# Optimization experiments

Hardware: AMD Instinct MI355X
Metric: run time of the kernel (lower is better)

Reference implementation:

```python
import jax, jax.numpy as jnp
import numpy as np
import math
from jax import lax

# cfg['MODEL'] constants
MU = 0.1          # FISTA step size
LMBD = 0.1        # LAMBDA[0], sparsity weight
N_DICT = 1        # EXPANSION_FACTOR
N_STEPS = 6       # NUM_LAYERS (FISTA iterations)
K = 3             # kernel_size
PAD = 1           # padding
STRIDE = 1        # stride (POOLING=False, stride passed to conv)
DN = ('NCHW', 'OIHW', 'NCHW')


def _conv(x, w):
    # F.conv2d(x, w, stride=1, padding=PAD)
    return lax.conv_general_dilated(x, w, (STRIDE, STRIDE), [(PAD, PAD), (PAD, PAD)], dimension_numbers=DN)


def _conv_t(y, w):
    # F.conv_transpose2d(y, w, stride=1, padding=PAD) == conv2d with flipped, in/out-swapped kernel, pad K-1-PAD
    wt = jnp.transpose(jnp.flip(w, (-1, -2)), (1, 0, 2, 3))  # [Cin, Cout, K, K]
    p = K - 1 - PAD
    return lax.conv_general_dilated(y, wt, (1, 1), [(p, p), (p, p)], dimension_numbers=DN)


def _shrink(z, thr):
    # non_negative=True soft-threshold: relu(z - thr)
    return jax.nn.relu(z - thr)


def setup_inputs() -> dict:
    key = jax.random.key(0)
    k1, k2 = jax.random.split(key)
    x = jax.random.normal(k1, (16, 64, 56, 56), dtype=jnp.float32)
    # dictionary weight [out_channels, in_channels*n_dict, K, K], kaiming-ish scale
    W = jax.random.normal(k2, (128, 64 * N_DICT, K, K), dtype=jnp.float32) * 0.05
    return {"x": x, "W": W}


def reference(x, W):
    # w_norm: each output filter normalized to unit Frobenius norm
    Wn = W / jnp.sqrt(jnp.sum(W * W, axis=(1, 2, 3), keepdims=True) + 1e-12)
    thr = MU * LMBD
    xr = jnp.tile(x, (1, N_DICT, 1, 1)) if N_DICT > 1 else x

    # FISTA iteration 0: c = shrink(mu * D^T x)
    c = _shrink(MU * _conv(xr, Wn), thr)
    y = c
    c_prev = c
    t = 1.0
    for _ in range(N_STEPS - 1):
        r = xr - _conv_t(y, Wn)                       # residual x - D c
        c_new = _shrink(y + MU * _conv(r, Wn), thr)   # gradient step + shrink
        t_next = (1.0 + math.sqrt(1.0 + 4.0 * t * t)) / 2.0
        y = c_new + ((t - 1.0) / t_next) * (c_new - c_prev)  # momentum
        c_prev = c_new
        t = t_next
    # POOLING=False -> DictConv2d returns the sparse code directly
    return c_prev
```

## Files before the change

kernel.cpp:

```cpp
#include <hip/hip_runtime.h>
#include <hip/hip_bf16.h>
#include <math.h>

typedef __attribute__((ext_vector_type(8))) short short8;
typedef __attribute__((ext_vector_type(4))) float f32x4;

#define MU_  0.1f
#define THR_ 0.01f

static __device__ inline short f2bf(float f) {
    __hip_bfloat16 h = __float2bfloat16(f);
    return *reinterpret_cast<short*>(&h);
}
static __device__ inline float bf2f(unsigned short u) {
    unsigned int x = ((unsigned int)u) << 16;
    return __builtin_bit_cast(float, x);
}

__global__ __launch_bounds__(256) void zero_kernel(float4* p, int n4) {
    int i = blockIdx.x * 256 + threadIdx.x;
    if (i < n4) p[i] = make_float4(0.f, 0.f, 0.f, 0.f);
}

__global__ __launch_bounds__(64) void wnorm_pack(
    const float* __restrict__ W, short* __restrict__ Wf2, short* __restrict__ Wt2) {
    int co = blockIdx.x, ci = threadIdx.x;
    const float* wp = W + (co * 64 + ci) * 9;
    float v[9]; float s = 0.f;
#pragma unroll
    for (int t = 0; t < 9; ++t) { v[t] = wp[t]; s += v[t] * v[t]; }
#pragma unroll
    for (int off = 32; off; off >>= 1) s += __shfl_xor(s, off, 64);
    float inv = 1.0f / sqrtf(s + 1e-12f);
#pragma unroll
    for (int t = 0; t < 9; ++t) {
        Wf2[((t * 8 + (ci >> 3)) * 128 + co) * 8 + (ci & 7)] = f2bf(v[t] * inv);
        Wt2[((t * 16 + (co >> 3)) * 64 + ci) * 8 + (co & 7)] = f2bf(v[8 - t] * inv);
    }
}

__global__ __launch_bounds__(256) void pack_x(
    const float* __restrict__ x, short* __restrict__ Xp) {
    __shared__ float lx[64 * 57];
    int row = blockIdx.x, n = blockIdx.y, tid = threadIdx.x;
    short* dst = Xp + ((size_t)(n * 58 + row) * 68) * 64;
    if (row >= 1 && row <= 56) {
        int h = row - 1;
        for (int j = tid; j < 64 * 56; j += 256) {
            int ci = j / 56, w = j - ci * 56;
            lx[ci * 57 + w] = x[((size_t)(n * 64 + ci)) * 3136 + h * 56 + w];
        }
        __syncthreads();
        for (int j = tid; j < 68 * 64; j += 256) {
            int s = j >> 6, ci = j & 63;
            float val = (s >= 2 && s < 58) ? lx[ci * 57 + (s - 2)] : 0.f;
            dst[(s << 6) + (ci ^ ((s & 7) << 3))] = f2bf(val);
        }
    } else {
        for (int j = tid; j < 68 * 64; j += 256) dst[j] = 0;
    }
}

__global__ __launch_bounds__(256) void conv_fwd(
    const short* __restrict__ inp,
    const short* __restrict__ Wf2,
    short* __restrict__ Yp,
    short* __restrict__ Cp,
    float* __restrict__ outp, int mode, float beta) {
    __shared__ __align__(16) short smem[14688];
    const int r = blockIdx.x + 1, cb = blockIdx.y, n = blockIdx.z, tid = threadIdx.x;
    {
        const short8* src = (const short8*)(inp + ((size_t)(n * 58 + (r - 1)) * 68) * 64);
        for (int j = tid; j < 1632; j += 256) {
            int srow = j >> 3, w = j & 7;
            *(short8*)(smem + srow * 72 + w * 8) = src[j];
        }
    }
    const int lane = tid & 63, ct = tid >> 6, quad = lane >> 4, l15 = lane & 15;
    const int co = cb * 64 + ct * 16 + l15;

    short8 Areg[18];
#pragma unroll
    for (int f = 0; f < 18; ++f) {
        int t = f >> 1, half = f & 1;
        Areg[f] = *(const short8*)(Wf2 + ((size_t)((t * 8 + half * 4 + quad) * 128 + co)) * 8);
    }
    __syncthreads();

    f32x4 acc[4];
#pragma unroll
    for (int pt = 0; pt < 4; ++pt) acc[pt] = (f32x4){0.f, 0.f, 0.f, 0.f};

#pragma unroll
    for (int f = 0; f < 18; ++f) {
        const int t = f >> 1, half = f & 1;
        const int dh = t / 3, dw = t % 3;
        const int u = l15 + dw + 1;
        const int phys = (half * 4 + quad) ^ (u & 7);
        const int base = (dh * 68 + u) * 72 + phys * 8;
#pragma unroll
        for (int pt = 0; pt < 4; ++pt) {
            short8 bv = *(const short8*)(smem + base + pt * 1152);
            acc[pt] = __builtin_amdgcn_mfma_f32_16x16x32_bf16(Areg[f], bv, acc[pt], 0, 0, 0);
        }
    }

    __syncthreads();
    short* tb_y = smem;
    short* tb_c = smem + 4608;
    const size_t prow = ((size_t)(n * 58 + r) * 68) * 128;
    if (mode != 0) {
        for (int item = tid; item < 448; item += 256) {
            int vv = item >> 3, g = item & 7;
            int s = vv + 2;
            size_t off = prow + (size_t)s * 128 + 8 * ((g + 8 * cb) ^ (s & 7));
            int o = vv * 72 + 8 * (g ^ (vv & 3));
            *(short8*)(tb_y + o) = *(const short8*)(Yp + off);
            if (mode == 1) *(short8*)(tb_c + o) = *(const short8*)(Cp + off);
        }
    }
    __syncthreads();
    const int h = r - 1;
#pragma unroll
    for (int pt = 0; pt < 4; ++pt) {
        const int px = pt * 16 + l15;
#pragma unroll
        for (int reg = 0; reg < 4; ++reg) {
            const int lch = ct * 16 + quad * 4 + reg;
            const int slot = px * 72 + (lch ^ ((px & 3) << 3));
            const float a = acc[pt][reg];
            if (mode == 0) {
                float c = fmaxf(MU_ * a - THR_, 0.f);
                short cb16 = f2bf(c);
                tb_y[slot] = cb16;
                tb_c[slot] = cb16;
            } else if (mode == 1) {
                float yold = bf2f((unsigned short)tb_y[slot]);
                float cold = bf2f((unsigned short)tb_c[slot]);
                float c = fmaxf(yold + MU_ * a - THR_, 0.f);
                tb_y[slot] = f2bf(c + beta * (c - cold));
                tb_c[slot] = f2bf(c);
            } else {
                if (px < 56) {
                    float yold = bf2f((unsigned short)tb_y[slot]);
                    float c = fmaxf(yold + MU_ * a - THR_, 0.f);
                    outp[((size_t)(n * 128 + cb * 64 + lch)) * 3136 + h * 56 + px] = c;
                }
            }
        }
    }
    if (mode != 2) {
        __syncthreads();
        for (int item = tid; item < 448; item += 256) {
            int vv = item >> 3, g = item & 7;
            int so = vv * 72 + 8 * (g ^ (vv & 3));
            short8 yv = *(const short8*)(tb_y + so);
            short8 cv = *(const short8*)(tb_c + so);
            int s = vv + 2;
            size_t off = prow + (size_t)s * 128 + 8 * ((g + 8 * cb) ^ (s & 7));
            *(short8*)(Yp + off) = yv;
            *(short8*)(Cp + off) = cv;
        }
    }
}

__global__ __launch_bounds__(256) void conv_t(
    const short* __restrict__ Ypb,
    const short* __restrict__ Wt2,
    const short* __restrict__ Xp,
    short* __restrict__ Rp) {
    __shared__ __align__(16) short smem[14688];
    const int r = blockIdx.x + 1, n = blockIdx.y, tid = threadIdx.x;
    const int lane = tid & 63, ct = tid >> 6, quad = lane >> 4, l15 = lane & 15;
    const int ci = ct * 16 + l15;
    const short8* src = (const short8*)(Ypb + ((size_t)(n * 58 + (r - 1)) * 68) * 128);

    f32x4 acc[4];
#pragma unroll
    for (int pt = 0; pt < 4; ++pt) acc[pt] = (f32x4){0.f, 0.f, 0.f, 0.f};

#pragma unroll
    for (int p = 0; p < 2; ++p) {
        if (p) __syncthreads();
        for (int j = tid; j < 1632; j += 256) {
            int srow = j >> 3, w = j & 7;
            *(short8*)(smem + srow * 72 + w * 8) = src[srow * 16 + p * 8 + w];
        }
        short8 Areg[18];
#pragma unroll
        for (int f = 0; f < 18; ++f) {
            int t = f >> 1, sh = f & 1;
            Areg[f] = *(const short8*)(Wt2 +
                ((size_t)((t * 16 + (p * 2 + sh) * 4 + quad) * 64 + ci)) * 8);
        }
        __syncthreads();
#pragma unroll
        for (int f = 0; f < 18; ++f) {
            const int t = f >> 1, sh = f & 1;
            const int dh = t / 3, dw = t % 3;
            const int u = l15 + dw + 1;
            const int phys = (sh * 4 + quad) ^ (u & 7);
            const int base = (dh * 68 + u) * 72 + phys * 8;
#pragma unroll
            for (int pt = 0; pt < 4; ++pt) {
                short8 bv = *(const short8*)(smem + base + pt * 1152);
                acc[pt] = __builtin_amdgcn_mfma_f32_16x16x32_bf16(Areg[f], bv, acc[pt], 0, 0, 0);
            }
        }
    }

    __syncthreads();
    short* tb = smem;
    const size_t prow = ((size_t)(n * 58 + r) * 68) * 64;
    for (int item = tid; item < 448; item += 256) {
        int vv = item >> 3, g = item & 7;
        int s = vv + 2;
        *(short8*)(tb + vv * 72 + 8 * (g ^ (vv & 3))) =
            *(const short8*)(Xp + prow + (size_t)s * 64 + 8 * (g ^ (s & 7)));
    }
    __syncthreads();
#pragma unroll
    for (int pt = 0; pt < 4; ++pt) {
        const int px = pt * 16 + l15;
#pragma unroll
        for (int reg = 0; reg < 4; ++reg) {
            const int cir = ct * 16 + quad * 4 + reg;
            const int slot = px * 72 + (cir ^ ((px & 3) << 3));
            float xo = bf2f((unsigned short)tb[slot]);
            tb[slot] = f2bf(xo - acc[pt][reg]);
        }
    }
    __syncthreads();
    for (int item = tid; item < 448; item += 256) {
        int vv = item >> 3, g = item & 7;
        short8 val = *(const short8*)(tb + vv * 72 + 8 * (g ^ (vv & 3)));
        int s = vv + 2;
        *(short8*)(Rp + prow + (size_t)s * 64 + 8 * (g ^ (s & 7))) = val;
    }
}

extern "C" void kernel_launch(void* const* d_in, const int* in_sizes, int n_in,
                              void* d_out, int out_size, void* d_ws, size_t ws_size,
                              hipStream_t stream) {
    const float* x = (const float*)d_in[0];
    const float* W = (const float*)d_in[1];
    float* out = (float*)d_out;

    const size_t XPN = (size_t)16 * 58 * 68 * 64;
    const size_t YPN = 2 * XPN;
    short* Xp = (short*)d_ws;
    short* Rp = Xp + XPN;
    short* Yp = Rp + XPN;
    short* Cp = Yp + YPN;
    short* Wf2 = Cp + YPN;
    short* Wt2 = Wf2 + 73728;

    const int n4 = (int)((XPN + YPN) * 2 / 16);
    hipLaunchKernelGGL(zero_kernel, dim3((n4 + 255) / 256), dim3(256), 0, stream,
                       (float4*)Rp, n4);
    hipLaunchKernelGGL(wnorm_pack, dim3(128), dim3(64), 0, stream, W, Wf2, Wt2);
    hipLaunchKernelGGL(pack_x, dim3(58, 16), dim3(256), 0, stream, x, Xp);

    dim3 gf(56, 2, 16), gt(56, 16), b(256, 1, 1);
    hipLaunchKernelGGL(conv_fwd, gf, b, 0, stream, Xp, Wf2, Yp, Cp,
                       (float*)nullptr, 0, 0.f);
    double t = 1.0;
    for (int it = 1; it <= 5; ++it) {
        hipLaunchKernelGGL(conv_t, gt, b, 0, stream, Yp, Wt2, Xp, Rp);
        double tn = (1.0 + sqrt(1.0 + 4.0 * t * t)) / 2.0;
        float beta = (float)((t - 1.0) / tn);
        hipLaunchKernelGGL(conv_fwd, gf, b, 0, stream, Rp, Wf2, Yp, Cp,
                           (it == 5) ? out : (float*)nullptr, (it == 5) ? 2 : 1,
                           beta);
        t = tn;
    }
}
```

Measured before the change: 372.4 us.

## Process two output rows per block in convs and fuse prep kernels

Each conv_fwd and conv_t block now computes two output rows instead of one. It stages four input rows in shared memory so the three-row halo is shared between them, and the register-held weights are reused across both rows. The Y and X epilogue loads are issued before the MFMA loop so their latency overlaps compute. The zeroing, weight-normalisation and x-packing kernels are merged into one launch. The grid is halved, which cuts the occupancy available to hide latency, and the extra accumulators and shared memory increase register and LDS pressure.

```diff
diff --git a/kernel.cpp b/kernel.cpp
--- a/kernel.cpp
+++ b/kernel.cpp
@@ -17,47 +17,51 @@
     return __builtin_bit_cast(float, x);
 }
 
-__global__ __launch_bounds__(256) void zero_kernel(float4* p, int n4) {
-    int i = blockIdx.x * 256 + threadIdx.x;
-    if (i < n4) p[i] = make_float4(0.f, 0.f, 0.f, 0.f);
-}
-
-__global__ __launch_bounds__(64) void wnorm_pack(
-    const float* __restrict__ W, short* __restrict__ Wf2, short* __restrict__ Wt2) {
-    int co = blockIdx.x, ci = threadIdx.x;
-    const float* wp = W + (co * 64 + ci) * 9;
-    float v[9]; float s = 0.f;
-#pragma unroll
-    for (int t = 0; t < 9; ++t) { v[t] = wp[t]; s += v[t] * v[t]; }
-#pragma unroll
-    for (int off = 32; off; off >>= 1) s += __shfl_xor(s, off, 64);
-    float inv = 1.0f / sqrtf(s + 1e-12f);
-#pragma unroll
-    for (int t = 0; t < 9; ++t) {
-        Wf2[((t * 8 + (ci >> 3)) * 128 + co) * 8 + (ci & 7)] = f2bf(v[t] * inv);
-        Wt2[((t * 16 + (co >> 3)) * 64 + ci) * 8 + (co & 7)] = f2bf(v[8 - t] * inv);
-    }
-}
-
-__global__ __launch_bounds__(256) void pack_x(
-    const float* __restrict__ x, short* __restrict__ Xp) {
+#define ZB_ 5916
+
+__global__ __launch_bounds__(256) void prep_kernel(
+    const float* __restrict__ x, const float* __restrict__ W,
+    float4* __restrict__ zbase, int n4,
+    short* __restrict__ Xp, short* __restrict__ Wf2, short* __restrict__ Wt2) {
     __shared__ float lx[64 * 57];
-    int row = blockIdx.x, n = blockIdx.y, tid = threadIdx.x;
-    short* dst = Xp + ((size_t)(n * 58 + row) * 68) * 64;
-    if (row >= 1 && row <= 56) {
-        int h = row - 1;
-        for (int j = tid; j < 64 * 56; j += 256) {
-            int ci = j / 56, w = j - ci * 56;
-            lx[ci * 57 + w] = x[((size_t)(n * 64 + ci)) * 3136 + h * 56 + w];
-        }
-        __syncthreads();
-        for (int j = tid; j < 68 * 64; j += 256) {
-            int s = j >> 6, ci = j & 63;
-            float val = (s >= 2 && s < 58) ? lx[ci * 57 + (s - 2)] : 0.f;
-            dst[(s << 6) + (ci ^ ((s & 7) << 3))] = f2bf(val);
+    const int bid = blockIdx.x, tid = threadIdx.x;
+    if (bid < ZB_) {
+        int i = bid * 256 + tid;
+        if (i < n4) zbase[i] = make_float4(0.f, 0.f, 0.f, 0.f);
+    } else if (bid < ZB_ + 32) {
+        int co = (bid - ZB_) * 4 + (tid >> 6);
+        int ci = tid & 63;
+        const float* wp = W + (co * 64 + ci) * 9;
+        float v[9]; float s = 0.f;
+#pragma unroll
+        for (int t = 0; t < 9; ++t) { v[t] = wp[t]; s += v[t] * v[t]; }
+#pragma unroll
+        for (int off = 32; off; off >>= 1) s += __shfl_xor(s, off, 64);
+        float inv = 1.0f / sqrtf(s + 1e-12f);
+#pragma unroll
+        for (int t = 0; t < 9; ++t) {
+            Wf2[((t * 8 + (ci >> 3)) * 128 + co) * 8 + (ci & 7)] = f2bf(v[t] * inv);
+            Wt2[((t * 16 + (co >> 3)) * 64 + ci) * 8 + (co & 7)] = f2bf(v[8 - t] * inv);
         }
     } else {
-        for (int j = tid; j < 68 * 64; j += 256) dst[j] = 0;
+        int pb = bid - ZB_ - 32;
+        int row = pb % 58, n = pb / 58;
+        short* dst = Xp + ((size_t)(n * 58 + row) * 68) * 64;
+        if (row >= 1 && row <= 56) {
+            int h = row - 1;
+            for (int j = tid; j < 64 * 56; j += 256) {
+                int ci = j / 56, w = j - ci * 56;
+                lx[ci * 57 + w] = x[((size_t)(n * 64 + ci)) * 3136 + h * 56 + w];
+            }
+            __syncthreads();
+            for (int j = tid; j < 68 * 64; j += 256) {
+                int s = j >> 6, ci = j & 63;
+                float val = (s >= 2 && s < 58) ? lx[ci * 57 + (s - 2)] : 0.f;
+                dst[(s << 6) + (ci ^ ((s & 7) << 3))] = f2bf(val);
+            }
+        } else {
+            for (int j = tid; j < 68 * 64; j += 256) dst[j] = 0;
+        }
     }
 }
 
@@ -67,17 +71,34 @@
     short* __restrict__ Yp,
     short* __restrict__ Cp,
     float* __restrict__ outp, int mode, float beta) {
-    __shared__ __align__(16) short smem[14688];
-    const int r = blockIdx.x + 1, cb = blockIdx.y, n = blockIdx.z, tid = threadIdx.x;
+    __shared__ __align__(16) short smem[19584];
+    const int r0 = blockIdx.x * 2 + 1, cb = blockIdx.y, n = blockIdx.z, tid = threadIdx.x;
     {
-        const short8* src = (const short8*)(inp + ((size_t)(n * 58 + (r - 1)) * 68) * 64);
-        for (int j = tid; j < 1632; j += 256) {
+        const short8* src = (const short8*)(inp + ((size_t)(n * 58 + (r0 - 1)) * 68) * 64);
+        for (int j = tid; j < 2176; j += 256) {
             int srow = j >> 3, w = j & 7;
             *(short8*)(smem + srow * 72 + w * 8) = src[j];
         }
     }
     const int lane = tid & 63, ct = tid >> 6, quad = lane >> 4, l15 = lane & 15;
     const int co = cb * 64 + ct * 16 + l15;
+    const size_t prow0 = ((size_t)(n * 58 + r0) * 68) * 128;
+
+    short8 yold8[4];
+    if (mode != 0) {
+#pragma unroll
+        for (int k = 0; k < 4; ++k) {
+            int item = tid + k * 256;
+            if (item < 896) {
+                int rr = item >= 448;
+                int rem = item - rr * 448;
+                int vv = rem >> 3, g = rem & 7;
+                int s = vv + 2;
+                yold8[k] = *(const short8*)(Yp + prow0 + (size_t)rr * 8704 +
+                                            (size_t)s * 128 + 8 * ((g + 8 * cb) ^ (s & 7)));
+            }
+        }
+    }
 
     short8 Areg[18];
 #pragma unroll
@@ -87,9 +108,11 @@
     }
     __syncthreads();
 
-    f32x4 acc[4];
-#pragma unroll
-    for (int pt = 0; pt < 4; ++pt) acc[pt] = (f32x4){0.f, 0.f, 0.f, 0.f};
+    f32x4 acc[2][4];
+#pragma unroll
+    for (int rr = 0; rr < 2; ++rr)
+#pragma unroll
+        for (int pt = 0; pt < 4; ++pt) acc[rr][pt] = (f32x4){0.f, 0.f, 0.f, 0.f};
 
 #pragma unroll
     for (int f = 0; f < 18; ++f) {
@@ -97,67 +120,86 @@
         const int dh = t / 3, dw = t % 3;
         const int u = l15 + dw + 1;
         const int phys = (half * 4 + quad) ^ (u & 7);
-        const int base = (dh * 68 + u) * 72 + phys * 8;
+        const int cbase = u * 72 + phys * 8;
+#pragma unroll
+        for (int rr = 0; rr < 2; ++rr) {
+            const int base = (rr + dh) * 4896 + cbase;
+#pragma unroll
+            for (int pt = 0; pt < 4; ++pt) {
+                short8 bv = *(const short8*)(smem + base + pt * 1152);
+                acc[rr][pt] = __builtin_amdgcn_mfma_f32_16x16x32_bf16(Areg[f], bv, acc[rr][pt], 0, 0, 0);
+            }
+        }
+    }
+
+    __syncthreads();
+    short* tb_y = smem;
+    short* tb_c = smem + 9216;
+    if (mode != 0) {
+#pragma unroll
+        for (int k = 0; k < 4; ++k) {
+            int item = tid + k * 256;
+            if (item < 896) {
+                int rr = item >= 448;
+                int rem = item - rr * 448;
+                int vv = rem >> 3, g = rem & 7;
+                int o = rr * 4608 + vv * 72 + 8 * (g ^ (vv & 3));
+                *(short8*)(tb_y + o) = yold8[k];
+                if (mode == 1) {
+                    int s = vv + 2;
+                    size_t off = prow0 + (size_t)rr * 8704 + (size_t)s * 128 +
+                                 8 * ((g + 8 * cb) ^ (s & 7));
+                    *(short8*)(tb_c + o) = *(const short8*)(Cp + off);
+                }
+            }
+        }
+    }
+    __syncthreads();
+    const int h0 = r0 - 1;
+#pragma unroll
+    for (int rr = 0; rr < 2; ++rr) {
 #pragma unroll
         for (int pt = 0; pt < 4; ++pt) {
-            short8 bv = *(const short8*)(smem + base + pt * 1152);
-            acc[pt] = __builtin_amdgcn_mfma_f32_16x16x32_bf16(Areg[f], bv, acc[pt], 0, 0, 0);
-        }
-    }
-
-    __syncthreads();
-    short* tb_y = smem;
-    short* tb_c = smem + 4608;
-    const size_t prow = ((size_t)(n * 58 + r) * 68) * 128;
-    if (mode != 0) {
-        for (int item = tid; item < 448; item += 256) {
-            int vv = item >> 3, g = item & 7;
-            int s = vv + 2;
-            size_t off = prow + (size_t)s * 128 + 8 * ((g + 8 * cb) ^ (s & 7));
-            int o = vv * 72 + 8 * (g ^ (vv & 3));
-            *(short8*)(tb_y + o) = *(const short8*)(Yp + off);
-            if (mode == 1) *(short8*)(tb_c + o) = *(const short8*)(Cp + off);
-        }
-    }
-    __syncthreads();
-    const int h = r - 1;
-#pragma unroll
-    for (int pt = 0; pt < 4; ++pt) {
-        const int px = pt * 16 + l15;
-#pragma unroll
-        for (int reg = 0; reg < 4; ++reg) {
-            const int lch = ct * 16 + quad * 4 + reg;
-            const int slot = px * 72 + (lch ^ ((px & 3) << 3));
-            const float a = acc[pt][reg];
-            if (mode == 0) {
-                float c = fmaxf(MU_ * a - THR_, 0.f);
-                short cb16 = f2bf(c);
-                tb_y[slot] = cb16;
-                tb_c[slot] = cb16;
-            } else if (mode == 1) {
-                float yold = bf2f((unsigned short)tb_y[slot]);
-                float cold = bf2f((unsigned short)tb_c[slot]);
-                float c = fmaxf(yold + MU_ * a - THR_, 0.f);
-                tb_y[slot] = f2bf(c + beta * (c - cold));
-                tb_c[slot] = f2bf(c);
-            } else {
-                if (px < 56) {
+            const int px = pt * 16 + l15;
+#pragma unroll
+            for (int reg = 0; reg < 4; ++reg) {
+                const int lch = ct * 16 + quad * 4 + reg;
+                const int slot = rr * 4608 + px * 72 + (lch ^ ((px & 3) << 3));
+                const float a = acc[rr][pt][reg];
+                if (mode == 0) {
+                    float c = fmaxf(MU_ * a - THR_, 0.f);
+                    short cb16 = f2bf(c);
+                    tb_y[slot] = cb16;
+                    tb_c[slot] = cb16;
+                } else if (mode == 1) {
                     float yold = bf2f((unsigned short)tb_y[slot]);
+                    float cold = bf2f((unsigned short)tb_c[slot]);
                     float c = fmaxf(yold + MU_ * a - THR_, 0.f);
-                    outp[((size_t)(n * 128 + cb * 64 + lch)) * 3136 + h * 56 + px] = c;
+                    tb_y[slot] = f2bf(c + beta * (c - cold));
+                    tb_c[slot] = f2bf(c);
+                } else {
+                    if (px < 56) {
+                        float yold = bf2f((unsigned short)tb_y[slot]);
+                        float c = fmaxf(yold + MU_ * a - THR_, 0.f);
+                        outp[((size_t)(n * 128 + cb * 64 + lch)) * 3136 +
+                             (h0 + rr) * 56 + px] = c;
+                    }
                 }
             }
         }
     }
     if (mode != 2) {
         __syncthreads();
-        for (int item = tid; item < 448; item += 256) {
-            int vv = item >> 3, g = item & 7;
-            int so = vv * 72 + 8 * (g ^ (vv & 3));
+        for (int item = tid; item < 896; item += 256) {
+            int rr = item >= 448;
+            int rem = item - rr * 448;
+            int vv = rem >> 3, g = rem & 7;
+            int so = rr * 4608 + vv * 72 + 8 * (g ^ (vv & 3));
             short8 yv = *(const short8*)(tb_y + so);
             short8 cv = *(const short8*)(tb_c + so);
             int s = vv + 2;
-            size_t off = prow + (size_t)s * 128 + 8 * ((g + 8 * cb) ^ (s & 7));
+            size_t off = prow0 + (size_t)rr * 8704 + (size_t)s * 128 +
+                         8 * ((g + 8 * cb) ^ (s & 7));
             *(short8*)(Yp + off) = yv;
             *(short8*)(Cp + off) = cv;
         }
@@ -169,20 +211,37 @@
     const short* __restrict__ Wt2,
     const short* __restrict__ Xp,
     short* __restrict__ Rp) {
-    __shared__ __align__(16) short smem[14688];
-    const int r = blockIdx.x + 1, n = blockIdx.y, tid = threadIdx.x;
+    __shared__ __align__(16) short smem[19584];
+    const int r0 = blockIdx.x * 2 + 1, n = blockIdx.y, tid = threadIdx.x;
     const int lane = tid & 63, ct = tid >> 6, quad = lane >> 4, l15 = lane & 15;
     const int ci = ct * 16 + l15;
-    const short8* src = (const short8*)(Ypb + ((size_t)(n * 58 + (r - 1)) * 68) * 128);
-
-    f32x4 acc[4];
-#pragma unroll
-    for (int pt = 0; pt < 4; ++pt) acc[pt] = (f32x4){0.f, 0.f, 0.f, 0.f};
+    const short8* src = (const short8*)(Ypb + ((size_t)(n * 58 + (r0 - 1)) * 68) * 128);
+    const size_t prow0 = ((size_t)(n * 58 + r0) * 68) * 64;
+
+    short8 xold8[4];
+#pragma unroll
+    for (int k = 0; k < 4; ++k) {
+        int item = tid + k * 256;
+        if (item < 896) {
+            int rr = item >= 448;
+            int rem = item - rr * 448;
+            int vv = rem >> 3, g = rem & 7;
+            int s = vv + 2;
+            xold8[k] = *(const short8*)(Xp + prow0 + (size_t)rr * 4352 +
+                                        (size_t)s * 64 + 8 * (g ^ (s & 7)));
+        }
+    }
+
+    f32x4 acc[2][4];
+#pragma unroll
+    for (int rr = 0; rr < 2; ++rr)
+#pragma unroll
+        for (int pt = 0; pt < 4; ++pt) acc[rr][pt] = (f32x4){0.f, 0.f, 0.f, 0.f};
 
 #pragma unroll
     for (int p = 0; p < 2; ++p) {
         if (p) __syncthreads();
-        for (int j = tid; j < 1632; j += 256) {
+        for (int j = tid; j < 2176; j += 256) {
             int srow = j >> 3, w = j & 7;
             *(short8*)(smem + srow * 72 + w * 8) = src[srow * 16 + p * 8 + w];
         }
@@ -200,42 +259,54 @@
             const int dh = t / 3, dw = t % 3;
             const int u = l15 + dw + 1;
             const int phys = (sh * 4 + quad) ^ (u & 7);
-            const int base = (dh * 68 + u) * 72 + phys * 8;
-#pragma unroll
-            for (int pt = 0; pt < 4; ++pt) {
-                short8 bv = *(const short8*)(smem + base + pt * 1152);
-                acc[pt] = __builtin_amdgcn_mfma_f32_16x16x32_bf16(Areg[f], bv, acc[pt], 0, 0, 0);
+            const int cbase = u * 72 + phys * 8;
+#pragma unroll
+            for (int rr = 0; rr < 2; ++rr) {
+                const int base = (rr + dh) * 4896 + cbase;
+#pragma unroll
+                for (int pt = 0; pt < 4; ++pt) {
+                    short8 bv = *(const short8*)(smem + base + pt * 1152);
+                    acc[rr][pt] = __builtin_amdgcn_mfma_f32_16x16x32_bf16(Areg[f], bv, acc[rr][pt], 0, 0, 0);
+                }
             }
         }
     }
 
     __syncthreads();
     short* tb = smem;
-    const size_t prow = ((size_t)(n * 58 + r) * 68) * 64;
-    for (int item = tid; item < 448; item += 256) {
-        int vv = item >> 3, g = item & 7;
+#pragma unroll
+    for (int k = 0; k < 4; ++k) {
+        int item = tid + k * 256;
+        if (item < 896) {
+            int rr = item >= 448;
+            int rem = item - rr * 448;
+            int vv = rem >> 3, g = rem & 7;
+            *(short8*)(tb + rr * 4608 + vv * 72 + 8 * (g ^ (vv & 3))) = xold8[k];
+        }
+    }
+    __syncthreads();
+#pragma unroll
+    for (int rr = 0; rr < 2; ++rr) {
+#pragma unroll
+        for (int pt = 0; pt < 4; ++pt) {
+            const int px = pt * 16 + l15;
+#pragma unroll
+            for (int reg = 0; reg < 4; ++reg) {
+                const int cir = ct * 16 + quad * 4 + reg;
+                const int slot = rr * 4608 + px * 72 + (cir ^ ((px & 3) << 3));
+                float xo = bf2f((unsigned short)tb[slot]);
+                tb[slot] = f2bf(xo - acc[rr][pt][reg]);
+            }
+        }
+    }
+    __syncthreads();
+    for (int item = tid; item < 896; item += 256) {
+        int rr = item >= 448;
+        int rem = item - rr * 448;
+        int vv = rem >> 3, g = rem & 7;
+        short8 val = *(const short8*)(tb + rr * 4608 + vv * 72 + 8 * (g ^ (vv & 3)));
         int s = vv + 2;
-        *(short8*)(tb + vv * 72 + 8 * (g ^ (vv & 3))) =
-            *(const short8*)(Xp + prow + (size_t)s * 64 + 8 * (g ^ (s & 7)));
-    }
-    __syncthreads();
-#pragma unroll
-    for (int pt = 0; pt < 4; ++pt) {
-        const int px = pt * 16 + l15;
-#pragma unroll
-        for (int reg = 0; reg < 4; ++reg) {
-            const int cir = ct * 16 + quad * 4 + reg;
-            const int slot = px * 72 + (cir ^ ((px & 3) << 3));
-            float xo = bf2f((unsigned short)tb[slot]);
-            tb[slot] = f2bf(xo - acc[pt][reg]);
-        }
-    }
-    __syncthreads();
-    for (int item = tid; item < 448; item += 256) {
-        int vv = item >> 3, g = item & 7;
-        short8 val = *(const short8*)(tb + vv * 72 + 8 * (g ^ (vv & 3)));
-        int s = vv + 2;
-        *(short8*)(Rp + prow + (size_t)s * 64 + 8 * (g ^ (s & 7))) = val;
+        *(short8*)(Rp + prow0 + (size_t)rr * 4352 + (size_t)s * 64 + 8 * (g ^ (s & 7))) = val;
     }
 }
 
@@ -256,12 +327,11 @@
     short* Wt2 = Wf2 + 73728;
 
     const int n4 = (int)((XPN + YPN) * 2 / 16);
-    hipLaunchKernelGGL(zero_kernel, dim3((n4 + 255) / 256), dim3(256), 0, stream,
-                       (float4*)Rp, n4);
-    hipLaunchKernelGGL(wnorm_pack, dim3(128), dim3(64), 0, stream, W, Wf2, Wt2);
-    hipLaunchKernelGGL(pack_x, dim3(58, 16), dim3(256), 0, stream, x, Xp);
-
-    dim3 gf(56, 2, 16), gt(56, 16), b(256, 1, 1);
+    const int prep_blocks = ZB_ + 32 + 58 * 16;
+    hipLaunchKernelGGL(prep_kernel, dim3(prep_blocks), dim3(256), 0, stream,
+                       x, W, (float4*)Rp, n4, Xp, Wf2, Wt2);
+
+    dim3 gf(28, 2, 16), gt(28, 16), b(256, 1, 1);
     hipLaunchKernelGGL(conv_fwd, gf, b, 0, stream, Xp, Wf2, Yp, Cp,
                        (float*)nullptr, 0, 0.f);
     double t = 1.0;
```

Measured after the change: 387.7 us. 4.1% more time.
